# Performance work log

Hardware: AMD Instinct MI355X
Metric: run time of the kernel (lower is better)

## Reference

```python
import jax, jax.numpy as jnp
import numpy as np

N = 100000      # n_nodes
E = 1600000     # n_edges (avg degree 16)
IN_C = 256
OUT_C = 64
HID = OUT_C * 2  # 128


def setup_inputs() -> dict:
    key = jax.random.key(0)
    k = jax.random.split(key, 4)
    x = jax.random.normal(k[0], (N, IN_C), dtype=jnp.float32)
    edge_index = jax.random.randint(k[1], (2, E), 0, N, dtype=jnp.int64)
    W1 = jax.random.normal(k[2], (IN_C, HID), dtype=jnp.float32) * (1.0 / np.sqrt(IN_C))
    b1 = jnp.zeros((HID,), dtype=jnp.float32)
    W2 = jax.random.normal(k[3], (HID, OUT_C), dtype=jnp.float32) * (1.0 / np.sqrt(HID))
    b2 = jnp.zeros((OUT_C,), dtype=jnp.float32)
    return {"x": x, "edge_index": edge_index, "W1": W1, "b1": b1, "W2": W2, "b2": b2}


def reference(x, edge_index, W1, b1, W2, b2):
    n = x.shape[0]
    # GCNConv default: add self-loops, symmetric normalization D^-1/2 A D^-1/2
    loop = jnp.arange(n, dtype=edge_index.dtype)
    src = jnp.concatenate([edge_index[0], loop])  # [E+N]
    dst = jnp.concatenate([edge_index[1], loop])  # [E+N]
    deg = jax.ops.segment_sum(jnp.ones_like(dst, dtype=x.dtype), dst, num_segments=n)
    dis = jax.lax.rsqrt(deg)  # deg >= 1 thanks to self-loops
    norm = dis[src] * dis[dst]  # [E+N]

    def gcn_conv(h, W, b):
        h = h @ W                                   # [n, d_out] dense transform first
        msg = h[src] * norm[:, None]                # [E+N, d_out] gather + scale
        return jax.ops.segment_sum(msg, dst, num_segments=n) + b

    h = jax.nn.relu(gcn_conv(x, W1, b1))
    return gcn_conv(h, W2, b2)
```

## Files before the change

kernel.cpp:

```cpp
#include <hip/hip_runtime.h>
#include <hip/hip_bf16.h>


#define GCN_IN_C 256
#define GCN_HID  128
#define GCN_OUT  64

#define BKT_SHIFT 8
#define BKT_NODES 256
#define EPB 4096

typedef __bf16 bf16x8 __attribute__((ext_vector_type(8)));
typedef __bf16 bf16x4 __attribute__((ext_vector_type(4)));
typedef float f32x4 __attribute__((ext_vector_type(4)));

__global__ __launch_bounds__(256) void k_bucket_hist(const int* __restrict__ dst,
                                                     int* __restrict__ bcnt, int e, int nb) {
  __shared__ int h[512];
  int tid = threadIdx.x;
  h[tid] = 0; h[tid + 256] = 0;
  __syncthreads();
  int base = blockIdx.x * EPB;
#pragma unroll
  for (int j = 0; j < EPB / 256; ++j) {
    int i = base + j * 256 + tid;
    if (i < e) atomicAdd(&h[dst[i] >> BKT_SHIFT], 1);
  }
  __syncthreads();
  if (tid < nb && h[tid]) atomicAdd(&bcnt[tid], h[tid]);
  if (tid + 256 < nb && h[tid + 256]) atomicAdd(&bcnt[tid + 256], h[tid + 256]);
}

__global__ __launch_bounds__(512) void k_scan_buckets(const int* __restrict__ bcnt,
                                                      int* __restrict__ bbase,
                                                      int* __restrict__ bcur, int nb) {
  __shared__ int sh[512];
  int t = threadIdx.x;
  int v = (t < nb) ? bcnt[t] : 0;
  sh[t] = v;
  __syncthreads();
  for (int d = 1; d < 512; d <<= 1) {
    int x = (t >= d) ? sh[t - d] : 0;
    __syncthreads();
    sh[t] += x;
    __syncthreads();
  }
  if (t < nb) {
    int ex = sh[t] - v;
    bbase[t] = ex;
    bcur[t] = ex;
  }
}

__global__ __launch_bounds__(256) void k_partition(const int* __restrict__ src,
                                                   const int* __restrict__ dst,
                                                   int* __restrict__ bcur,
                                                   unsigned int* __restrict__ part,
                                                   int e, int nb) {
  __shared__ int h[512];
  __shared__ int base[512];
  int tid = threadIdx.x;
  h[tid] = 0; h[tid + 256] = 0;
  __syncthreads();
  int b0 = blockIdx.x * EPB;
  int s[EPB / 256], d[EPB / 256], rk[EPB / 256];
#pragma unroll
  for (int j = 0; j < EPB / 256; ++j) {
    int i = b0 + j * 256 + tid;
    if (i < e) {
      s[j] = src[i];
      d[j] = dst[i];
      rk[j] = atomicAdd(&h[d[j] >> BKT_SHIFT], 1);
    }
  }
  __syncthreads();
  if (tid < nb && h[tid]) base[tid] = atomicAdd(&bcur[tid], h[tid]);
  if (tid + 256 < nb && h[tid + 256]) base[tid + 256] = atomicAdd(&bcur[tid + 256], h[tid + 256]);
  __syncthreads();
#pragma unroll
  for (int j = 0; j < EPB / 256; ++j) {
    int i = b0 + j * 256 + tid;
    if (i < e) {
      int bk = d[j] >> BKT_SHIFT;
      unsigned int dl = (unsigned int)(d[j] & (BKT_NODES - 1));
      part[base[bk] + rk[j]] = (dl << 24) | (unsigned int)s[j];
    }
  }
}

__global__ __launch_bounds__(256) void k_bucket_csr(
    const unsigned int* __restrict__ part, const int* __restrict__ bbase,
    const int* __restrict__ bcnt, int* __restrict__ off, int* __restrict__ end,
    float* __restrict__ dis, int* __restrict__ csr, int n) {
  __shared__ int cnt[256];
  __shared__ int sc[256];
  __shared__ int cur[256];
  int b = blockIdx.x, tid = threadIdx.x;
  int node0 = b << BKT_SHIFT;
  int eb0 = bbase[b];
  int ebn = bcnt[b];
  cnt[tid] = 0;
  __syncthreads();
  for (int i = tid; i < ebn; i += 256) atomicAdd(&cnt[part[eb0 + i] >> 24], 1);
  __syncthreads();
  int v = cnt[tid];
  sc[tid] = v;
  __syncthreads();
  for (int dd = 1; dd < 256; dd <<= 1) {
    int x = (tid >= dd) ? sc[tid - dd] : 0;
    __syncthreads();
    sc[tid] += x;
    __syncthreads();
  }
  int lo = sc[tid] - v;
  cur[tid] = lo;
  int node = node0 + tid;
  if (node < n) {
    off[node] = eb0 + lo;
    end[node] = eb0 + lo + v;
    dis[node] = rsqrtf((float)v + 1.0f);
  }
  __syncthreads();
  for (int i = tid; i < ebn; i += 256) {
    unsigned int u = part[eb0 + i];
    int r = atomicAdd(&cur[u >> 24], 1);
    csr[eb0 + r] = (int)(u & 0xFFFFFFu);
  }
}

__global__ __launch_bounds__(256) void k_split_w_all(
    const float* __restrict__ W1, __bf16* __restrict__ w1hi,
    __bf16* __restrict__ w1lo2,
    const float* __restrict__ W2, __bf16* __restrict__ w2sp) {
  constexpr int N1 = (GCN_IN_C / 32) * 4 * GCN_HID;
  constexpr int N2 = (GCN_HID / 32) * 4 * GCN_OUT;
  int idx = blockIdx.x * 256 + threadIdx.x;
  if (idx < N1) {
    int n = idx % GCN_HID;
    int g = (idx / GCN_HID) & 3;
    int ks = idx / (4 * GCN_HID);
    __bf16* hi = w1hi + (size_t)ks * (4 * GCN_HID * 8) + ((size_t)g * GCN_HID + n) * 8;
    __bf16* lo = w1lo2 + (((size_t)ks * (GCN_HID / 16) + (n >> 4)) * 64 + g * 16 + (n & 15)) * 8;
#pragma unroll
    for (int j = 0; j < 8; ++j) {
      float f = W1[(size_t)(ks * 32 + g * 8 + j) * GCN_HID + n];
      __bf16 h = (__bf16)f;
      hi[j] = h;
      lo[j] = (__bf16)(f - (float)h);
    }
  } else if (idx < N1 + N2) {
    int i2 = idx - N1;
    int n = i2 % GCN_OUT;
    int g = (i2 / GCN_OUT) & 3;
    int ks = i2 / (4 * GCN_OUT);
    __bf16* hi = w2sp + (size_t)ks * (2 * 4 * GCN_OUT * 8) + ((size_t)g * GCN_OUT + n) * 8;
    __bf16* lo = hi + 4 * GCN_OUT * 8;
#pragma unroll
    for (int j = 0; j < 8; ++j) {
      float f = W2[(size_t)(ks * 32 + g * 8 + j) * GCN_OUT + n];
      __bf16 h = (__bf16)f;
      hi[j] = h;
      lo[j] = (__bf16)(f - (float)h);
    }
  }
}

template<int K, int NOUT>
__global__ __launch_bounds__(512, 4) void k_gemm_l1(
    const float* __restrict__ X, const __bf16* __restrict__ Whi,
    const __bf16* __restrict__ Wlo, const float* __restrict__ dis,
    __bf16* __restrict__ T, int M) {
  constexpr int KSTEPS = K / 32;
  constexpr int NF = NOUT / 16;
  constexpr int HI = 4 * NOUT * 8;
  __shared__ __bf16 lds[KSTEPS * HI];

  const int tid = threadIdx.x;
  const int wave = tid >> 6;
  const int lane = tid & 63;
  const int l15 = lane & 15;
  const int lg = lane >> 4;
  const int r0w = blockIdx.x * 128 + wave * 16;

  {
#pragma unroll
    for (int i = 0; i < KSTEPS * HI * 2 / (512 * 16); ++i) {
      const char* gs = (const char*)Whi + ((size_t)i * 512 + tid) * 16;
      char* ls = (char*)lds + (size_t)i * 8192 + wave * 1024 + lane * 16;
      __builtin_amdgcn_global_load_lds(
          (const __attribute__((address_space(1))) void*)gs,
          (__attribute__((address_space(3))) void*)ls, 16, 0, 0);
    }
  }

  f32x4 acc[NF];
#pragma unroll
  for (int nf = 0; nf < NF; ++nf) acc[nf] = (f32x4){0.f, 0.f, 0.f, 0.f};

  int row = r0w + l15;
  int rowA = (row < M) ? row : (M - 1);
  const int boff = lg * NOUT * 8 + l15 * 8;

  __syncthreads();

#pragma unroll 1
  for (int ks = 0; ks < KSTEPS; ++ks) {
    const float* ap = X + (size_t)rowA * K + ks * 32 + lg * 8;
    float4 a0 = *(const float4*)ap;
    float4 a1 = *(const float4*)(ap + 4);
    bf16x8 bl[NF];
#pragma unroll
    for (int nf = 0; nf < NF; ++nf)
      bl[nf] = *(const bf16x8*)(Wlo + (((size_t)ks * NF + nf) * 64 + lane) * 8);
    bf16x8 ah, al;
    {
      float va[8] = {a0.x, a0.y, a0.z, a0.w, a1.x, a1.y, a1.z, a1.w};
#pragma unroll
      for (int j = 0; j < 8; ++j) {
        __bf16 h = (__bf16)va[j];
        ah[j] = h;
        al[j] = (__bf16)(va[j] - (float)h);
      }
    }
    const __bf16* lh = lds + (size_t)ks * HI + boff;
#pragma unroll
    for (int nf = 0; nf < NF; ++nf) {
      bf16x8 bh = *(const bf16x8*)(lh + nf * 128);
      acc[nf] = __builtin_amdgcn_mfma_f32_16x16x32_bf16(bh, ah, acc[nf], 0, 0, 0);
      acc[nf] = __builtin_amdgcn_mfma_f32_16x16x32_bf16(bl[nf], ah, acc[nf], 0, 0, 0);
      acc[nf] = __builtin_amdgcn_mfma_f32_16x16x32_bf16(bh, al, acc[nf], 0, 0, 0);
    }
  }

  if (row < M) {
    float dv = dis[row];
#pragma unroll
    for (int nf = 0; nf < NF; ++nf) {
      bf16x4 pk;
#pragma unroll
      for (int r = 0; r < 4; ++r) pk[r] = (__bf16)(dv * acc[nf][r]);
      *(bf16x4*)(T + (size_t)row * NOUT + nf * 16 + lg * 4) = pk;
    }
  }
}

template<int K, int NOUT>
__global__ __launch_bounds__(256) void k_gemm_l2(
    const __bf16* __restrict__ A, const __bf16* __restrict__ Wsp,
    const float* __restrict__ dis, __bf16* __restrict__ T, int M) {
  constexpr int KSTEPS = K / 32;
  constexpr int NF = NOUT / 16;
  constexpr int TILE = 2 * 4 * NOUT * 8;
  constexpr int HL = 4 * NOUT * 8;
  __shared__ __bf16 lds[KSTEPS * TILE];

  const int tid = threadIdx.x;
  const int wave = tid >> 6;
  const int lane = tid & 63;
  const int l15 = lane & 15;
  const int lg = lane >> 4;
  const int r0w = blockIdx.x * 64 + wave * 16;

  {
    constexpr int CHUNKS = KSTEPS * TILE * 2 / 1024;
#pragma unroll
    for (int it = 0; it < CHUNKS / 4; ++it) {
      int c = it * 4 + wave;
      const char* gs = (const char*)Wsp + c * 1024 + lane * 16;
      char* ls = (char*)lds + c * 1024;
      __builtin_amdgcn_global_load_lds(
          (const __attribute__((address_space(1))) void*)gs,
          (__attribute__((address_space(3))) void*)ls, 16, 0, 0);
    }
  }

  f32x4 acc[NF];
#pragma unroll
  for (int nf = 0; nf < NF; ++nf) acc[nf] = (f32x4){0.f, 0.f, 0.f, 0.f};

  int row = r0w + l15;
  int rowA = (row < M) ? row : (M - 1);
  const int boff = lg * NOUT * 8 + l15 * 8;

  bf16x8 ca, na;
  ca = *(const bf16x8*)(A + (size_t)rowA * K + lg * 8);
  __syncthreads();

#pragma unroll 1
  for (int ks = 0; ks < KSTEPS; ++ks) {
    if (ks + 1 < KSTEPS)
      na = *(const bf16x8*)(A + (size_t)rowA * K + (ks + 1) * 32 + lg * 8);
    const __bf16* lh = lds + (size_t)ks * TILE + boff;
    const __bf16* ll = lh + HL;
#pragma unroll
    for (int nf = 0; nf < NF; ++nf) {
      bf16x8 bh = *(const bf16x8*)(lh + nf * 128);
      bf16x8 bl = *(const bf16x8*)(ll + nf * 128);
      acc[nf] = __builtin_amdgcn_mfma_f32_16x16x32_bf16(bh, ca, acc[nf], 0, 0, 0);
      acc[nf] = __builtin_amdgcn_mfma_f32_16x16x32_bf16(bl, ca, acc[nf], 0, 0, 0);
    }
    ca = na;
  }

  if (row < M) {
    float dv = dis[row];
#pragma unroll
    for (int nf = 0; nf < NF; ++nf) {
      bf16x4 pk;
#pragma unroll
      for (int r = 0; r < 4; ++r) pk[r] = (__bf16)(dv * acc[nf][r]);
      *(bf16x4*)(T + (size_t)row * NOUT + nf * 16 + lg * 4) = pk;
    }
  }
}

template<int C, bool RELU, typename OutT>
__global__ __launch_bounds__(256) void k_agg_csr(
    const int* __restrict__ csr, const int* __restrict__ off,
    const int* __restrict__ end, const __bf16* __restrict__ ts,
    const float* __restrict__ dis, const float* __restrict__ bias,
    OutT* __restrict__ out, int n) {
  constexpr int LPG = C / 8;
  int gtid = blockIdx.x * 256 + threadIdx.x;
  int node = gtid / LPG;
  int gl = gtid % LPG;
  if (node >= n) return;

  float acc[8];
  {
    bf16x8 v = *(const bf16x8*)(ts + (size_t)node * C + gl * 8);
#pragma unroll
    for (int j = 0; j < 8; ++j) acc[j] = (float)v[j];
  }

  int e = off[node];
  int e1 = end[node];
  for (; e + 4 <= e1; e += 4) {
    int s0 = csr[e];
    int s1 = csr[e + 1];
    int s2 = csr[e + 2];
    int s3 = csr[e + 3];
    bf16x8 v0 = *(const bf16x8*)(ts + (size_t)s0 * C + gl * 8);
    bf16x8 v1 = *(const bf16x8*)(ts + (size_t)s1 * C + gl * 8);
    bf16x8 v2 = *(const bf16x8*)(ts + (size_t)s2 * C + gl * 8);
    bf16x8 v3 = *(const bf16x8*)(ts + (size_t)s3 * C + gl * 8);
#pragma unroll
    for (int j = 0; j < 8; ++j)
      acc[j] += ((float)v0[j] + (float)v1[j]) + ((float)v2[j] + (float)v3[j]);
  }
  for (; e < e1; ++e) {
    int s0 = csr[e];
    bf16x8 v0 = *(const bf16x8*)(ts + (size_t)s0 * C + gl * 8);
#pragma unroll
    for (int j = 0; j < 8; ++j) acc[j] += (float)v0[j];
  }

  float di = dis[node];
  float o[8];
#pragma unroll
  for (int j = 0; j < 8; ++j) {
    o[j] = di * acc[j] + bias[gl * 8 + j];
    if (RELU) o[j] = fmaxf(o[j], 0.f);
  }
  if constexpr (sizeof(OutT) == 2) {
    bf16x8 pv;
#pragma unroll
    for (int j = 0; j < 8; ++j) pv[j] = (__bf16)o[j];
    *(bf16x8*)((__bf16*)out + (size_t)node * C + gl * 8) = pv;
  } else {
    float4* op = (float4*)((float*)out + (size_t)node * C + gl * 8);
    op[0] = make_float4(o[0], o[1], o[2], o[3]);
    op[1] = make_float4(o[4], o[5], o[6], o[7]);
  }
}

extern "C" void kernel_launch(void* const* d_in, const int* in_sizes, int n_in,
                              void* d_out, int out_size, void* d_ws, size_t ws_size,
                              hipStream_t stream) {
  const float* x  = (const float*)d_in[0];
  const int*   ei = (const int*)d_in[1];
  const float* W1 = (const float*)d_in[2];
  const float* b1 = (const float*)d_in[3];
  const float* W2 = (const float*)d_in[4];
  const float* b2 = (const float*)d_in[5];
  float* out = (float*)d_out;

  const int N = in_sizes[0] / GCN_IN_C;
  const int E = in_sizes[1] / 2;
  const int* src = ei;
  const int* dst = ei + E;
  const int NB = (N + BKT_NODES - 1) >> BKT_SHIFT;
  const int EB = (E + EPB - 1) / EPB;

  char* p = (char*)d_ws;
  float* dis = (float*)p;             p += (size_t)N * 4;
  __bf16* t1s = (__bf16*)p;           p += (size_t)N * GCN_HID * 2;
  __bf16* a1  = (__bf16*)p;           p += (size_t)N * GCN_HID * 2;
  int* off   = (int*)p;               p += (size_t)N * 4;
  int* end   = (int*)p;               p += (size_t)N * 4;
  int* csr   = (int*)p;               p += (size_t)E * 4;
  int* bcnt  = (int*)p;               p += 512 * 4;
  int* bbase = (int*)p;               p += 512 * 4;
  int* bcur  = (int*)p;               p += 512 * 4;
  __bf16* w1hi  = (__bf16*)p;         p += (size_t)(GCN_IN_C / 32) * 4 * GCN_HID * 8 * 2;
  __bf16* w1lo2 = (__bf16*)p;         p += (size_t)(GCN_IN_C / 32) * 4 * GCN_HID * 8 * 2;
  __bf16* w2sp  = (__bf16*)p;
  unsigned int* part = (unsigned int*)a1;
  __bf16* t2s = t1s;

  k_split_w_all<<<(4096 + 1024 + 255) / 256, 256, 0, stream>>>(W1, w1hi, w1lo2, W2, w2sp);
  hipMemsetAsync(bcnt, 0, 512 * sizeof(int), stream);

  k_bucket_hist<<<EB, 256, 0, stream>>>(dst, bcnt, E, NB);
  k_scan_buckets<<<1, 512, 0, stream>>>(bcnt, bbase, bcur, NB);
  k_partition<<<EB, 256, 0, stream>>>(src, dst, bcur, part, E, NB);
  k_bucket_csr<<<NB, 256, 0, stream>>>(part, bbase, bcnt, off, end, dis, csr, N);

  k_gemm_l1<GCN_IN_C, GCN_HID>
      <<<(N + 127) / 128, 512, 0, stream>>>(x, w1hi, w1lo2, dis, t1s, N);
  k_agg_csr<GCN_HID, true, __bf16>
      <<<((size_t)N * (GCN_HID / 8) + 255) / 256, 256, 0, stream>>>(csr, off, end, t1s, dis, b1, a1, N);

  k_gemm_l2<GCN_HID, GCN_OUT>
      <<<(N + 63) / 64, 256, 0, stream>>>(a1, w2sp, dis, t2s, N);
  k_agg_csr<GCN_OUT, false, float>
      <<<((size_t)N * (GCN_OUT / 8) + 255) / 256, 256, 0, stream>>>(csr, off, end, t2s, dis, b2, out, N);
}
```

Measured before the change: 207.5 us.

## Stage W1 low half in LDS and prefetch next A tile in layer-1 GEMM

```diff
diff --git a/kernel.cpp b/kernel.cpp
--- a/kernel.cpp
+++ b/kernel.cpp
@@ -166,14 +166,15 @@
 }
 
 template<int K, int NOUT>
-__global__ __launch_bounds__(512, 4) void k_gemm_l1(
+__global__ __launch_bounds__(512, 2) void k_gemm_l1(
     const float* __restrict__ X, const __bf16* __restrict__ Whi,
     const __bf16* __restrict__ Wlo, const float* __restrict__ dis,
     __bf16* __restrict__ T, int M) {
   constexpr int KSTEPS = K / 32;
   constexpr int NF = NOUT / 16;
   constexpr int HI = 4 * NOUT * 8;
-  __shared__ __bf16 lds[KSTEPS * HI];
+  constexpr int HITOT = KSTEPS * HI;
+  extern __shared__ __bf16 lds[];
 
   const int tid = threadIdx.x;
   const int wave = tid >> 6;
@@ -184,13 +185,21 @@
 
   {
 #pragma unroll
-    for (int i = 0; i < KSTEPS * HI * 2 / (512 * 16); ++i) {
+    for (int i = 0; i < 8; ++i) {
       const char* gs = (const char*)Whi + ((size_t)i * 512 + tid) * 16;
       char* ls = (char*)lds + (size_t)i * 8192 + wave * 1024 + lane * 16;
       __builtin_amdgcn_global_load_lds(
           (const __attribute__((address_space(1))) void*)gs,
           (__attribute__((address_space(3))) void*)ls, 16, 0, 0);
     }
+#pragma unroll
+    for (int i = 0; i < 8; ++i) {
+      const char* gs = (const char*)Wlo + ((size_t)i * 512 + tid) * 16;
+      char* ls = (char*)lds + 65536 + (size_t)i * 8192 + wave * 1024 + lane * 16;
+      __builtin_amdgcn_global_load_lds(
+          (const __attribute__((address_space(1))) void*)gs,
+          (__attribute__((address_space(3))) void*)ls, 16, 0, 0);
+    }
   }
 
   f32x4 acc[NF];
@@ -201,20 +210,22 @@
   int rowA = (row < M) ? row : (M - 1);
   const int boff = lg * NOUT * 8 + l15 * 8;
 
+  auto loadA = [&](int ks, float4* v0, float4* v1) {
+    const float* ap = X + (size_t)rowA * K + ks * 32 + lg * 8;
+    *v0 = *(const float4*)ap;
+    *v1 = *(const float4*)(ap + 4);
+  };
+
+  float4 ca0, ca1, na0, na1;
+  loadA(0, &ca0, &ca1);
   __syncthreads();
 
 #pragma unroll 1
   for (int ks = 0; ks < KSTEPS; ++ks) {
-    const float* ap = X + (size_t)rowA * K + ks * 32 + lg * 8;
-    float4 a0 = *(const float4*)ap;
-    float4 a1 = *(const float4*)(ap + 4);
-    bf16x8 bl[NF];
-#pragma unroll
-    for (int nf = 0; nf < NF; ++nf)
-      bl[nf] = *(const bf16x8*)(Wlo + (((size_t)ks * NF + nf) * 64 + lane) * 8);
+    if (ks + 1 < KSTEPS) loadA(ks + 1, &na0, &na1);
     bf16x8 ah, al;
     {
-      float va[8] = {a0.x, a0.y, a0.z, a0.w, a1.x, a1.y, a1.z, a1.w};
+      float va[8] = {ca0.x, ca0.y, ca0.z, ca0.w, ca1.x, ca1.y, ca1.z, ca1.w};
 #pragma unroll
       for (int j = 0; j < 8; ++j) {
         __bf16 h = (__bf16)va[j];
@@ -223,13 +234,17 @@
       }
     }
     const __bf16* lh = lds + (size_t)ks * HI + boff;
+    const __bf16* ll = lds + HITOT + ((size_t)ks * NF * 64) * 8 + lane * 8;
 #pragma unroll
     for (int nf = 0; nf < NF; ++nf) {
       bf16x8 bh = *(const bf16x8*)(lh + nf * 128);
+      bf16x8 bl = *(const bf16x8*)(ll + (size_t)nf * 512);
       acc[nf] = __builtin_amdgcn_mfma_f32_16x16x32_bf16(bh, ah, acc[nf], 0, 0, 0);
-      acc[nf] = __builtin_amdgcn_mfma_f32_16x16x32_bf16(bl[nf], ah, acc[nf], 0, 0, 0);
+      acc[nf] = __builtin_amdgcn_mfma_f32_16x16x32_bf16(bl, ah, acc[nf], 0, 0, 0);
       acc[nf] = __builtin_amdgcn_mfma_f32_16x16x32_bf16(bh, al, acc[nf], 0, 0, 0);
     }
+    ca0 = na0;
+    ca1 = na1;
   }
 
   if (row < M) {
@@ -252,7 +267,7 @@
   constexpr int NF = NOUT / 16;
   constexpr int TILE = 2 * 4 * NOUT * 8;
   constexpr int HL = 4 * NOUT * 8;
-  __shared__ __bf16 lds[KSTEPS * TILE];
+  __shared__ __bf16 lds2[KSTEPS * TILE];
 
   const int tid = threadIdx.x;
   const int wave = tid >> 6;
@@ -267,7 +282,7 @@
     for (int it = 0; it < CHUNKS / 4; ++it) {
       int c = it * 4 + wave;
       const char* gs = (const char*)Wsp + c * 1024 + lane * 16;
-      char* ls = (char*)lds + c * 1024;
+      char* ls = (char*)lds2 + c * 1024;
       __builtin_amdgcn_global_load_lds(
           (const __attribute__((address_space(1))) void*)gs,
           (__attribute__((address_space(3))) void*)ls, 16, 0, 0);
@@ -290,7 +305,7 @@
   for (int ks = 0; ks < KSTEPS; ++ks) {
     if (ks + 1 < KSTEPS)
       na = *(const bf16x8*)(A + (size_t)rowA * K + (ks + 1) * 32 + lg * 8);
-    const __bf16* lh = lds + (size_t)ks * TILE + boff;
+    const __bf16* lh = lds2 + (size_t)ks * TILE + boff;
     const __bf16* ll = lh + HL;
 #pragma unroll
     for (int nf = 0; nf < NF; ++nf) {
@@ -417,7 +432,7 @@
   k_bucket_csr<<<NB, 256, 0, stream>>>(part, bbase, bcnt, off, end, dis, csr, N);
 
   k_gemm_l1<GCN_IN_C, GCN_HID>
-      <<<(N + 127) / 128, 512, 0, stream>>>(x, w1hi, w1lo2, dis, t1s, N);
+      <<<(N + 127) / 128, 512, 131072, stream>>>(x, w1hi, w1lo2, dis, t1s, N);
   k_agg_csr<GCN_HID, true, __bf16>
       <<<((size_t)N * (GCN_HID / 8) + 255) / 256, 256, 0, stream>>>(csr, off, end, t1s, dis, b1, a1, N);
 
```

Result: no change. 206.3 us (-0.6%).
